# Optimization experiments

Hardware: AMD Instinct MI355X
Metric: run time of the kernel (lower is better)

The kernel has to match this reference:

```python
import jax, jax.numpy as jnp
import numpy as np

SAMPLE_RATE = 48000
FREQ_MIN, FREQ_MAX = 20.0, 2000.0
MOD_MIN, MOD_MAX = -1.0, 2.0


def setup_inputs() -> dict:
    key = jax.random.key(0)
    k1, k2, k3 = jax.random.split(key, 3)
    B, N = 512, 65536
    freq = jax.random.uniform(k1, (B, 1), dtype=jnp.float32)
    mod_env = jax.random.uniform(k2, (B, N), dtype=jnp.float32)
    mod_amount = jax.random.uniform(k3, (B, 1), dtype=jnp.float32)
    return {"num_samples": N, "freq": freq, "mod_env": mod_env, "mod_amount": mod_amount}


def reference(num_samples, freq, mod_env, mod_amount):
    # de-normalize controls
    f0 = FREQ_MIN + (FREQ_MAX - FREQ_MIN) * freq            # [B, 1] Hz
    f0 = 2.0 * jnp.pi * f0 / SAMPLE_RATE                    # [B, 1] rad/sample
    mod_amt = MOD_MIN + (MOD_MAX - MOD_MIN) * mod_amount    # [B, 1]
    # instantaneous angular frequency per sample: f0 * (1 + mod_env * mod_amt)
    freq_env = f0 + mod_env * mod_amt * f0                  # [B, N]
    # prepend zero, cumsum, drop last -> exclusive prefix sum (phase)
    padded = jnp.concatenate([jnp.zeros_like(freq_env[:, :1]), freq_env], axis=-1)
    phase = jnp.cumsum(padded, axis=-1)[:, :-1]             # [B, N]
    return jnp.sin(phase)
```

## Files before the change

### kernel.cpp

```cpp
#include <hip/hip_runtime.h>


constexpr int BLOCK = 1024;
constexpr int VPT   = 8;

__global__ __launch_bounds__(BLOCK) void osc_kernel(
    const float* __restrict__ freq,
    const float* __restrict__ mod_env,
    const float* __restrict__ mod_amount,
    float* __restrict__ out,
    int N)
{
    const int row  = blockIdx.x;
    const int tid  = threadIdx.x;
    const int lane = tid & 63;
    const int wid  = tid >> 6;

    __shared__ double s_wsum[BLOCK / 64];
    __shared__ double s_woff[BLOCK / 64 + 1];

    const double f0rev = (20.0 + 1980.0 * (double)freq[row]) / 48000.0;
    const double amt   = -1.0 + 3.0 * (double)mod_amount[row];
    const double k     = f0rev * amt;

    const float* __restrict__ rowp = mod_env + (size_t)row * N;
    float* __restrict__ outp       = out     + (size_t)row * N;

    const int chunk  = BLOCK * VPT;
    const int nchunk = N / chunk;

    double carry = 0.0;

    const float* p0 = rowp + tid * VPT;
    float4 curA = *(const float4*)(p0);
    float4 curB = *(const float4*)(p0 + 4);

    for (int c = 0; c < nchunk; ++c) {
        float4 nxtA = curA, nxtB = curB;
        if (c + 1 < nchunk) {
            const float* p = rowp + (size_t)(c + 1) * chunk + tid * VPT;
            nxtA = *(const float4*)(p);
            nxtB = *(const float4*)(p + 4);
        }

        double v0 = fma((double)curA.x, k, f0rev);
        double v1 = fma((double)curA.y, k, f0rev);
        double v2 = fma((double)curA.z, k, f0rev);
        double v3 = fma((double)curA.w, k, f0rev);
        double v4 = fma((double)curB.x, k, f0rev);
        double v5 = fma((double)curB.y, k, f0rev);
        double v6 = fma((double)curB.z, k, f0rev);
        double v7 = fma((double)curB.w, k, f0rev);

        double tsum = ((v0 + v1) + (v2 + v3)) + ((v4 + v5) + (v6 + v7));

        double x = tsum;
        #pragma unroll
        for (int off = 1; off < 64; off <<= 1) {
            double y = __shfl_up(x, off, 64);
            if (lane >= off) x += y;
        }

        if (lane == 63) s_wsum[wid] = x;
        __syncthreads();

        if (tid < BLOCK / 64) {
            double w  = s_wsum[tid];
            double xs = w;
            #pragma unroll
            for (int off = 1; off < BLOCK / 64; off <<= 1) {
                double y = __shfl_up(xs, off, 64);
                if (tid >= off) xs += y;
            }
            s_woff[tid] = xs - w;
            if (tid == BLOCK / 64 - 1) s_woff[BLOCK / 64] = xs;
        }
        __syncthreads();

        double phase = carry + s_woff[wid] + (x - tsum);

        float4 oA, oB;
        {
            double pf;
            pf = phase - floor(phase); oA.x = __builtin_amdgcn_sinf((float)pf); phase += v0;
            pf = phase - floor(phase); oA.y = __builtin_amdgcn_sinf((float)pf); phase += v1;
            pf = phase - floor(phase); oA.z = __builtin_amdgcn_sinf((float)pf); phase += v2;
            pf = phase - floor(phase); oA.w = __builtin_amdgcn_sinf((float)pf); phase += v3;
            pf = phase - floor(phase); oB.x = __builtin_amdgcn_sinf((float)pf); phase += v4;
            pf = phase - floor(phase); oB.y = __builtin_amdgcn_sinf((float)pf); phase += v5;
            pf = phase - floor(phase); oB.z = __builtin_amdgcn_sinf((float)pf); phase += v6;
            pf = phase - floor(phase); oB.w = __builtin_amdgcn_sinf((float)pf); phase += v7;
        }

        float* q = outp + (size_t)c * chunk + tid * VPT;
        *(float4*)(q)     = oA;
        *(float4*)(q + 4) = oB;

        carry += s_woff[BLOCK / 64];
        __syncthreads();

        curA = nxtA; curB = nxtB;
    }
}

extern "C" void kernel_launch(void* const* d_in, const int* in_sizes, int n_in,
                              void* d_out, int out_size, void* d_ws, size_t ws_size,
                              hipStream_t stream) {
    const float* freq       = (const float*)d_in[1];
    const float* mod_env    = (const float*)d_in[2];
    const float* mod_amount = (const float*)d_in[3];
    float* out = (float*)d_out;

    const int B = in_sizes[1];
    const int N = in_sizes[2] / B;

    osc_kernel<<<B, BLOCK, 0, stream>>>(freq, mod_env, mod_amount, out, N);
}
```

Measured before the change: 45.79 us.

## Replace two-stage block scan with redundant per-wave scan and double-buffered sums

Every wave now reads all 16 wave totals from a double-buffered shared array and scans them itself with shuffles. This removes two of the three __syncthreads per chunk and the serial scan done by a single small group of threads. Output stores also become nontemporal to reduce cache pollution from the write-only stream. The cost is redundant shuffle work in every wave, and the double buffer must be safe against a wave overwriting a slot another wave is still reading.

After: 56.04 us. 1.22x slower.

```diff
diff --git a/kernel.cpp b/kernel.cpp
--- a/kernel.cpp
+++ b/kernel.cpp
@@ -3,6 +3,9 @@
 
 constexpr int BLOCK = 1024;
 constexpr int VPT   = 8;
+constexpr int NW    = BLOCK / 64;
+
+typedef float f32x4 __attribute__((ext_vector_type(4)));
 
 __global__ __launch_bounds__(BLOCK) void osc_kernel(
     const float* __restrict__ freq,
@@ -16,8 +19,7 @@
     const int lane = tid & 63;
     const int wid  = tid >> 6;
 
-    __shared__ double s_wsum[BLOCK / 64];
-    __shared__ double s_woff[BLOCK / 64 + 1];
+    __shared__ double s_wsum[2][NW];
 
     const double f0rev = (20.0 + 1980.0 * (double)freq[row]) / 48000.0;
     const double amt   = -1.0 + 3.0 * (double)mod_amount[row];
@@ -32,15 +34,15 @@
     double carry = 0.0;
 
     const float* p0 = rowp + tid * VPT;
-    float4 curA = *(const float4*)(p0);
-    float4 curB = *(const float4*)(p0 + 4);
+    f32x4 curA = *(const f32x4*)(p0);
+    f32x4 curB = *(const f32x4*)(p0 + 4);
 
     for (int c = 0; c < nchunk; ++c) {
-        float4 nxtA = curA, nxtB = curB;
+        f32x4 nxtA = curA, nxtB = curB;
         if (c + 1 < nchunk) {
             const float* p = rowp + (size_t)(c + 1) * chunk + tid * VPT;
-            nxtA = *(const float4*)(p);
-            nxtB = *(const float4*)(p + 4);
+            nxtA = *(const f32x4*)(p);
+            nxtB = *(const f32x4*)(p + 4);
         }
 
         double v0 = fma((double)curA.x, k, f0rev);
@@ -61,25 +63,23 @@
             if (lane >= off) x += y;
         }
 
-        if (lane == 63) s_wsum[wid] = x;
+        if (lane == 63) s_wsum[c & 1][wid] = x;
         __syncthreads();
 
-        if (tid < BLOCK / 64) {
-            double w  = s_wsum[tid];
-            double xs = w;
-            #pragma unroll
-            for (int off = 1; off < BLOCK / 64; off <<= 1) {
-                double y = __shfl_up(xs, off, 64);
-                if (tid >= off) xs += y;
-            }
-            s_woff[tid] = xs - w;
-            if (tid == BLOCK / 64 - 1) s_woff[BLOCK / 64] = xs;
+        double w = (lane < NW) ? s_wsum[c & 1][lane] : 0.0;
+        #pragma unroll
+        for (int off = 1; off < NW; off <<= 1) {
+            double y = __shfl_up(w, off, 64);
+            if (lane >= off) w += y;
         }
-        __syncthreads();
+        double total = __shfl(w, NW - 1, 64);
+        double exc   = __shfl(w, (wid > 0 ? wid - 1 : 0), 64);
+        if (wid == 0) exc = 0.0;
 
-        double phase = carry + s_woff[wid] + (x - tsum);
+        double phase = carry + exc + (x - tsum);
+        carry += total;
 
-        float4 oA, oB;
+        f32x4 oA, oB;
         {
             double pf;
             pf = phase - floor(phase); oA.x = __builtin_amdgcn_sinf((float)pf); phase += v0;
@@ -93,11 +93,8 @@
         }
 
         float* q = outp + (size_t)c * chunk + tid * VPT;
-        *(float4*)(q)     = oA;
-        *(float4*)(q + 4) = oB;
-
-        carry += s_woff[BLOCK / 64];
-        __syncthreads();
+        __builtin_nontemporal_store(oA, (f32x4*)(q));
+        __builtin_nontemporal_store(oB, (f32x4*)(q + 4));
 
         curA = nxtA; curB = nxtB;
     }
```
